# Kernel tuning notes

Hardware: AMD Instinct MI355X
Metric: run time of the kernel (lower is better)

Reference implementation:

```python
import jax, jax.numpy as jnp
import numpy as np

ZMAX = 92          # max atomic number in NLH table
BOHR = 0.52917721  # Bohr radius in Angstrom (au.BOHR)
ENERGY_UNIT = 1.0  # multiplier for 'Ha'
N_ATOMS = 100_000
N_EDGES = 6_400_000
TAB = (ZMAX + 1) ** 2  # 8649


def setup_inputs() -> dict:
    key = jax.random.key(0)
    k1, k2, k3, k4, k5, k6, k7 = jax.random.split(key, 7)
    species = jax.random.randint(k1, (N_ATOMS,), 0, 93, dtype=jnp.int32)
    edge_src = jax.random.randint(k2, (N_EDGES,), 0, N_ATOMS, dtype=jnp.int32)
    edge_dst = jax.random.randint(k3, (N_EDGES,), 0, N_ATOMS, dtype=jnp.int32)
    # distances kept away from zero (division by rijs)
    distances = 0.5 + 4.5 * jax.random.uniform(k4, (N_EDGES,), dtype=jnp.float32)
    switch = jax.random.uniform(k5, (N_EDGES,), dtype=jnp.float32)
    CS = jax.random.uniform(k6, (TAB, 3), dtype=jnp.float32)
    ALPHAS = jax.random.uniform(k7, (TAB, 3), dtype=jnp.float32) + 0.5
    return {"species": species, "edge_src": edge_src, "edge_dst": edge_dst,
            "distances": distances, "switch": switch, "CS": CS, "ALPHAS": ALPHAS}


def reference(species, edge_src, edge_dst, distances, switch, CS, ALPHAS):
    # pair index into (zmax+1)^2 coefficient table
    s12 = species[edge_src] + ZMAX * species[edge_dst]
    cs = CS[s12]          # [E, 3]
    alphas = ALPHAS[s12]  # [E, 3]
    Z = jnp.where(species > 0, species.astype(distances.dtype), 0.0)
    # 3-term exponential screening function
    phi = jnp.sum(cs * jnp.exp(-alphas * distances[:, None]), axis=-1)  # [E]
    ereppair = Z[edge_src] * Z[edge_dst] * phi * switch / distances
    erep_atomic = ENERGY_UNIT * 0.5 * BOHR * jax.ops.segment_sum(
        ereppair, edge_src, num_segments=species.shape[0])
    return erep_atomic
```

## Files before the change

kernel.cpp:

```cpp
#include <hip/hip_runtime.h>
#include <hip/hip_fp16.h>


#define ZMAX_C 92
#define TAB93  93
#define NTAB   (TAB93 * TAB93)
#define HALF_BOHR 0.264588605f
#define NBMAX 64
#define APB 2048
#define APB_LOG 11
#define SPLITS 16
#define TPB 256
#define EPT 8
#define BLK_EDGES (TPB * EPT)

typedef int            ivec4 __attribute__((ext_vector_type(4)));
typedef float          fvec4 __attribute__((ext_vector_type(4)));

#if __has_builtin(__builtin_amdgcn_rcpf)
#define FAST_RCP(x) __builtin_amdgcn_rcpf(x)
#else
#define FAST_RCP(x) (1.0f / (x))
#endif

__global__ __launch_bounds__(TPB) void p0_prep(
    const float* __restrict__ CS, const float* __restrict__ ALPHAS,
    const int* __restrict__ species,
    uint4* __restrict__ tab16, unsigned char* __restrict__ spc8,
    unsigned* __restrict__ cursor, float* __restrict__ out,
    int n_atoms, int nb)
{
    int i = blockIdx.x * TPB + threadIdx.x;
    if (i < NTAB) {
        int sd = i / TAB93;
        int ss = i - TAB93 * sd;
        int ref = ss + ZMAX_C * sd;
        float Z = (ss > 0 && sd > 0) ? (float)(ss * sd) : 0.0f;
        __half h[8];
        h[0] = __float2half_rn(CS[3*ref+0] * Z);
        h[1] = __float2half_rn(CS[3*ref+1] * Z);
        h[2] = __float2half_rn(CS[3*ref+2] * Z);
        h[3] = __float2half_rn(-ALPHAS[3*ref+0]);
        h[4] = __float2half_rn(-ALPHAS[3*ref+1]);
        h[5] = __float2half_rn(-ALPHAS[3*ref+2]);
        h[6] = __half(0.0f); h[7] = __half(0.0f);
        tab16[i] = *reinterpret_cast<uint4*>(h);
    }
    if (i < n_atoms) {
        spc8[i] = (unsigned char)species[i];
        out[i] = 0.0f;
    }
    if (i < nb) cursor[i] = 0u;
}

__device__ __forceinline__ float half_lo(unsigned u) {
    return __half2float(*reinterpret_cast<const __half*>(&u));
}
__device__ __forceinline__ float half_hi(unsigned u) {
    unsigned s = u >> 16;
    return __half2float(*reinterpret_cast<const __half*>(&s));
}

__global__ __launch_bounds__(TPB) void p1_bin(
    const int* __restrict__ edge_src, const int* __restrict__ edge_dst,
    const float* __restrict__ dist, const float* __restrict__ swt,
    const unsigned char* __restrict__ spc8, const uint4* __restrict__ tab16,
    unsigned* __restrict__ pairs, unsigned* __restrict__ cursor,
    int nb, int cap, int n_edges)
{
    __shared__ unsigned stage[BLK_EDGES];
    __shared__ unsigned hist4[4][NBMAX];
    __shared__ unsigned hist[NBMAX];
    __shared__ unsigned lbase[NBMAX];
    __shared__ unsigned gbase[NBMAX];

    int tid = threadIdx.x;
    if (tid < NBMAX) {
        hist4[0][tid] = 0; hist4[1][tid] = 0;
        hist4[2][tid] = 0; hist4[3][tid] = 0;
    }
    __syncthreads();

    int lane = tid & 63, wave = tid >> 6;
    long long wbase = (long long)blockIdx.x * BLK_EDGES + (long long)wave * (64 * EPT);

    unsigned meta[EPT];
    unsigned short s12r[EPT];

    {
        int srcv[EPT], dstv[EPT];
        #pragma unroll
        for (int j = 0; j < EPT / 4; ++j) {
            long long e0 = wbase + j * 256 + lane * 4;
            if (e0 + 3 < (long long)n_edges) {
                ivec4 s4 = *reinterpret_cast<const ivec4*>(edge_src + e0);
                ivec4 d4 = *reinterpret_cast<const ivec4*>(edge_dst + e0);
                #pragma unroll
                for (int k = 0; k < 4; ++k) { srcv[j*4+k] = s4[k]; dstv[j*4+k] = d4[k]; }
            } else {
                #pragma unroll
                for (int k = 0; k < 4; ++k) {
                    long long e = e0 + k;
                    bool v = (e < (long long)n_edges);
                    srcv[j*4+k] = v ? edge_src[e] : 0;
                    dstv[j*4+k] = v ? edge_dst[e] : 0;
                }
            }
        }
        int ssv[EPT], sdv[EPT];
        #pragma unroll
        for (int i = 0; i < EPT; ++i) ssv[i] = spc8[srcv[i]];
        #pragma unroll
        for (int i = 0; i < EPT; ++i) sdv[i] = spc8[dstv[i]];
        #pragma unroll
        for (int j = 0; j < EPT / 4; ++j) {
            long long e0 = wbase + j * 256 + lane * 4;
            #pragma unroll
            for (int k = 0; k < 4; ++k) {
                int idx = j * 4 + k;
                s12r[idx] = (unsigned short)(ssv[idx] + TAB93 * sdv[idx]);
                meta[idx] = 0u;
                if (e0 + k < (long long)n_edges) {
                    unsigned b    = (unsigned)srcv[idx] >> APB_LOG;
                    unsigned lsrc = (unsigned)srcv[idx] & (APB - 1);
                    unsigned rank = atomicAdd(&hist4[wave][b], 1u);
                    meta[idx] = 0x80000000u | (rank << 17) | (b << 11) | lsrc;
                }
            }
        }
    }
    __syncthreads();
    if (tid < 64) {
        unsigned h0 = hist4[0][tid], h1 = hist4[1][tid];
        unsigned h2 = hist4[2][tid], h3 = hist4[3][tid];
        unsigned tot = h0 + h1 + h2 + h3;
        hist4[0][tid] = 0;
        hist4[1][tid] = h0;
        hist4[2][tid] = h0 + h1;
        hist4[3][tid] = h0 + h1 + h2;
        if (tid < nb) hist[tid] = tot;
        unsigned v = (tid < nb) ? tot : 0u;
        unsigned x = v;
        #pragma unroll
        for (int off = 1; off < 64; off <<= 1) {
            unsigned y = __shfl_up(x, off);
            if ((tid & 63) >= off) x += y;
        }
        if (tid < nb) {
            lbase[tid] = x - v;
            gbase[tid] = v ? atomicAdd(cursor + tid, v) : 0u;
        }
    }
    __syncthreads();

    for (int jj = 0; jj < EPT / 8; ++jj) {
        long long eA = wbase + (jj*2+0) * 256 + lane * 4;
        long long eB = wbase + (jj*2+1) * 256 + lane * 4;
        float rA[4], wA[4], rB[4], wB[4];
        bool fullB = (eB + 3 < (long long)n_edges);
        if (fullB) {
            fvec4 r4 = *reinterpret_cast<const fvec4*>(dist + eA);
            fvec4 w4 = *reinterpret_cast<const fvec4*>(swt + eA);
            fvec4 r5 = *reinterpret_cast<const fvec4*>(dist + eB);
            fvec4 w5 = *reinterpret_cast<const fvec4*>(swt + eB);
            #pragma unroll
            for (int k = 0; k < 4; ++k) {
                rA[k] = r4[k]; wA[k] = w4[k]; rB[k] = r5[k]; wB[k] = w5[k];
            }
        } else {
            #pragma unroll
            for (int k = 0; k < 4; ++k) {
                long long ea = eA + k, eb = eB + k;
                bool va = (ea < (long long)n_edges), vb = (eb < (long long)n_edges);
                rA[k] = va ? dist[ea] : 1.f;  wA[k] = va ? swt[ea] : 0.f;
                rB[k] = vb ? dist[eb] : 1.f;  wB[k] = vb ? swt[eb] : 0.f;
            }
        }
        uint4 tA[4], tB[4];
        #pragma unroll
        for (int k = 0; k < 4; ++k) tA[k] = tab16[s12r[jj*8 + k]];
        #pragma unroll
        for (int k = 0; k < 4; ++k) tB[k] = tab16[s12r[jj*8 + 4 + k]];
        #pragma unroll
        for (int g = 0; g < 2; ++g) {
            const float* r = g ? rB : rA;
            const float* w = g ? wB : wA;
            const uint4* t = g ? tB : tA;
            #pragma unroll
            for (int k = 0; k < 4; ++k) {
                int idx = jj * 8 + g * 4 + k;
                unsigned m = meta[idx];
                if (!(m & 0x80000000u)) continue;
                float c0 = half_lo(t[k].x), c1 = half_hi(t[k].x);
                float c2 = half_lo(t[k].y), na0 = half_hi(t[k].y);
                float na1 = half_lo(t[k].z), na2 = half_hi(t[k].z);
                float phi = c0 * __expf(na0 * r[k])
                          + c1 * __expf(na1 * r[k])
                          + c2 * __expf(na2 * r[k]);
                float val = HALF_BOHR * phi * w[k] * FAST_RCP(r[k]);
                unsigned b = (m >> 11) & 63u;
                unsigned pos = lbase[b] + hist4[wave][b] + ((m >> 17) & 0x3FFFu);
                unsigned short hb = __half_as_ushort(__float2half_rn(val));
                stage[pos] = ((m & (APB - 1)) << 16) | (unsigned)hb;
            }
        }
    }
    __syncthreads();
    for (int b = wave; b < nb; b += 4) {
        unsigned cnt = hist[b], lb = lbase[b], gb = gbase[b];
        unsigned* dst = pairs + (size_t)b * (size_t)cap + gb;
        for (unsigned i = lane; i < cnt; i += 64)
            if (gb + i < (unsigned)cap) dst[i] = stage[lb + i];
    }
}

__global__ __launch_bounds__(TPB) void p2a_reduce(
    const unsigned* __restrict__ pairs, const unsigned* __restrict__ cursor,
    float* __restrict__ out, int cap, int n_atoms)
{
    int b = blockIdx.x / SPLITS;
    int s = blockIdx.x % SPLITS;
    __shared__ float acc[APB];
    for (int i = threadIdx.x; i < APB; i += TPB) acc[i] = 0.f;
    __syncthreads();
    unsigned cnt = cursor[b];
    if (cnt > (unsigned)cap) cnt = (unsigned)cap;
    unsigned nq = (cnt + 3u) >> 2;
    unsigned qb = (unsigned)((unsigned long long)nq * s / SPLITS);
    unsigned qe = (unsigned)((unsigned long long)nq * (s + 1) / SPLITS);
    const uint4* p4 = (const uint4*)(pairs + (size_t)b * (size_t)cap);
    for (unsigned q = qb + threadIdx.x; q < qe; q += TPB) {
        uint4 v = p4[q];
        unsigned base = q << 2;
        if (base + 3u < cnt) {
            unsafeAtomicAdd(&acc[v.x >> 16], __half2float(__ushort_as_half((unsigned short)(v.x & 0xFFFFu))));
            unsafeAtomicAdd(&acc[v.y >> 16], __half2float(__ushort_as_half((unsigned short)(v.y & 0xFFFFu))));
            unsafeAtomicAdd(&acc[v.z >> 16], __half2float(__ushort_as_half((unsigned short)(v.z & 0xFFFFu))));
            unsafeAtomicAdd(&acc[v.w >> 16], __half2float(__ushort_as_half((unsigned short)(v.w & 0xFFFFu))));
        } else {
            unsigned vv[4] = {v.x, v.y, v.z, v.w};
            #pragma unroll
            for (int e = 0; e < 4; ++e)
                if (base + (unsigned)e < cnt)
                    unsafeAtomicAdd(&acc[vv[e] >> 16],
                        __half2float(__ushort_as_half((unsigned short)(vv[e] & 0xFFFFu))));
        }
    }
    __syncthreads();
    int abase = b * APB;
    for (int k = threadIdx.x; k < APB; k += TPB) {
        int atom = abase + k;
        float vv = acc[k];
        if (atom < n_atoms && vv != 0.0f)
            unsafeAtomicAdd(&out[atom], vv);
    }
}

__global__ __launch_bounds__(TPB) void erep_edges_direct(
    const int* __restrict__ edge_src, const int* __restrict__ edge_dst,
    const float* __restrict__ dist, const float* __restrict__ swt,
    const int* __restrict__ species, const float* __restrict__ CS,
    const float* __restrict__ ALPHAS, float* __restrict__ out, int n_edges)
{
    int e = blockIdx.x * TPB + threadIdx.x;
    if (e >= n_edges) return;
    int ss = species[edge_src[e]], sd = species[edge_dst[e]];
    int prod = ss * sd;
    if (prod == 0) return;
    int s12 = ss + ZMAX_C * sd;
    float r = dist[e];
    float phi = CS[3*s12+0] * __expf(-ALPHAS[3*s12+0] * r)
              + CS[3*s12+1] * __expf(-ALPHAS[3*s12+1] * r)
              + CS[3*s12+2] * __expf(-ALPHAS[3*s12+2] * r);
    atomicAdd(out + edge_src[e],
              HALF_BOHR * (float)prod * phi * swt[e] * FAST_RCP(r));
}

extern "C" void kernel_launch(void* const* d_in, const int* in_sizes, int n_in,
                              void* d_out, int out_size, void* d_ws, size_t ws_size,
                              hipStream_t stream)
{
    const int*   species  = (const int*)  d_in[0];
    const int*   edge_src = (const int*)  d_in[1];
    const int*   edge_dst = (const int*)  d_in[2];
    const float* dist     = (const float*)d_in[3];
    const float* swt      = (const float*)d_in[4];
    const float* CS       = (const float*)d_in[5];
    const float* ALPHAS   = (const float*)d_in[6];
    float* out = (float*)d_out;

    int n_atoms = in_sizes[0];
    int n_edges = in_sizes[1];

    int nb = (n_atoms + APB - 1) / APB;
    long long capll = (long long)n_edges / nb + (long long)n_edges / ((long long)nb * 32) + 256;
    int cap = (int)((capll + 31) & ~31LL);

    size_t pairs_sz = ((size_t)nb * (size_t)cap * 4 + 255) & ~(size_t)255;
    size_t cur_sz   = ((size_t)nb * 4 + 255) & ~(size_t)255;
    size_t tab_sz   = ((size_t)NTAB * 16 + 255) & ~(size_t)255;
    size_t spc_sz   = ((size_t)n_atoms + 255) & ~(size_t)255;
    size_t need = pairs_sz + cur_sz + tab_sz + spc_sz;

    if (nb <= NBMAX && n_edges > 0 && ws_size >= need) {
        char* w = (char*)d_ws;
        unsigned*       pairs   = (unsigned*)w;
        unsigned*       cursor  = (unsigned*)(w + pairs_sz);
        uint4*          tab16   = (uint4*)(w + pairs_sz + cur_sz);
        unsigned char*  spc8    = (unsigned char*)(w + pairs_sz + cur_sz + tab_sz);

        int pmax = n_atoms > NTAB ? n_atoms : NTAB;
        p0_prep<<<(pmax + TPB - 1) / TPB, TPB, 0, stream>>>(
            CS, ALPHAS, species, tab16, spc8, cursor, out, n_atoms, nb);

        p1_bin<<<(n_edges + BLK_EDGES - 1) / BLK_EDGES, TPB, 0, stream>>>(
            edge_src, edge_dst, dist, swt, spc8, tab16,
            pairs, cursor, nb, cap, n_edges);

        p2a_reduce<<<nb * SPLITS, TPB, 0, stream>>>(pairs, cursor, out, cap, n_atoms);
    } else {
        (void)hipMemsetAsync(d_out, 0, (size_t)out_size * sizeof(float), stream);
        erep_edges_direct<<<(n_edges + TPB - 1) / TPB, TPB, 0, stream>>>(
            edge_src, edge_dst, dist, swt, species, CS, ALPHAS, out, n_edges);
    }
}
```

Measured before the change: 241.1 us.

## Stage packed coefficient table in LDS with 1024-thread binning blocks

Packs the per-pair coefficient table into 12-byte fp16 triples and copies the whole table into shared memory at the start of each binning block. Per-edge table lookups become LDS reads instead of global gathers. The block size grows to 1024 threads so the table load is shared across more edges, and the per-wave histogram and prefix logic is generalized to 16 waves. This costs a roughly 104 KB table copy per block and limits occupancy to about one block per CU.

```diff
diff --git a/kernel.cpp b/kernel.cpp
--- a/kernel.cpp
+++ b/kernel.cpp
@@ -10,7 +10,9 @@
 #define APB 2048
 #define APB_LOG 11
 #define SPLITS 16
-#define TPB 256
+#define TPB  1024
+#define NW   (TPB / 64)
+#define TPB2 256
 #define EPT 8
 #define BLK_EDGES (TPB * EPT)
 
@@ -23,28 +25,28 @@
 #define FAST_RCP(x) (1.0f / (x))
 #endif
 
-__global__ __launch_bounds__(TPB) void p0_prep(
+__global__ __launch_bounds__(TPB2) void p0_prep(
     const float* __restrict__ CS, const float* __restrict__ ALPHAS,
     const int* __restrict__ species,
-    uint4* __restrict__ tab16, unsigned char* __restrict__ spc8,
+    unsigned* __restrict__ tabp, unsigned char* __restrict__ spc8,
     unsigned* __restrict__ cursor, float* __restrict__ out,
     int n_atoms, int nb)
 {
-    int i = blockIdx.x * TPB + threadIdx.x;
+    int i = blockIdx.x * TPB2 + threadIdx.x;
     if (i < NTAB) {
         int sd = i / TAB93;
         int ss = i - TAB93 * sd;
         int ref = ss + ZMAX_C * sd;
         float Z = (ss > 0 && sd > 0) ? (float)(ss * sd) : 0.0f;
-        __half h[8];
-        h[0] = __float2half_rn(CS[3*ref+0] * Z);
-        h[1] = __float2half_rn(CS[3*ref+1] * Z);
-        h[2] = __float2half_rn(CS[3*ref+2] * Z);
-        h[3] = __float2half_rn(-ALPHAS[3*ref+0]);
-        h[4] = __float2half_rn(-ALPHAS[3*ref+1]);
-        h[5] = __float2half_rn(-ALPHAS[3*ref+2]);
-        h[6] = __half(0.0f); h[7] = __half(0.0f);
-        tab16[i] = *reinterpret_cast<uint4*>(h);
+        unsigned short h0 = __half_as_ushort(__float2half_rn(CS[3*ref+0] * Z));
+        unsigned short h1 = __half_as_ushort(__float2half_rn(CS[3*ref+1] * Z));
+        unsigned short h2 = __half_as_ushort(__float2half_rn(CS[3*ref+2] * Z));
+        unsigned short h3 = __half_as_ushort(__float2half_rn(-ALPHAS[3*ref+0]));
+        unsigned short h4 = __half_as_ushort(__float2half_rn(-ALPHAS[3*ref+1]));
+        unsigned short h5 = __half_as_ushort(__float2half_rn(-ALPHAS[3*ref+2]));
+        tabp[3*i+0] = (unsigned)h0 | ((unsigned)h1 << 16);
+        tabp[3*i+1] = (unsigned)h2 | ((unsigned)h3 << 16);
+        tabp[3*i+2] = (unsigned)h4 | ((unsigned)h5 << 16);
     }
     if (i < n_atoms) {
         spc8[i] = (unsigned char)species[i];
@@ -64,22 +66,22 @@
 __global__ __launch_bounds__(TPB) void p1_bin(
     const int* __restrict__ edge_src, const int* __restrict__ edge_dst,
     const float* __restrict__ dist, const float* __restrict__ swt,
-    const unsigned char* __restrict__ spc8, const uint4* __restrict__ tab16,
+    const unsigned char* __restrict__ spc8, const unsigned* __restrict__ tabp,
     unsigned* __restrict__ pairs, unsigned* __restrict__ cursor,
     int nb, int cap, int n_edges)
 {
+    __shared__ unsigned tabL[NTAB * 3];
     __shared__ unsigned stage[BLK_EDGES];
-    __shared__ unsigned hist4[4][NBMAX];
+    __shared__ unsigned histW[NW][NBMAX];
     __shared__ unsigned hist[NBMAX];
     __shared__ unsigned lbase[NBMAX];
     __shared__ unsigned gbase[NBMAX];
 
     int tid = threadIdx.x;
-    if (tid < NBMAX) {
-        hist4[0][tid] = 0; hist4[1][tid] = 0;
-        hist4[2][tid] = 0; hist4[3][tid] = 0;
-    }
-    __syncthreads();
+    ((unsigned*)histW)[tid] = 0;
+    __syncthreads();
+
+    for (int i = tid; i < NTAB * 3; i += TPB) tabL[i] = tabp[i];
 
     int lane = tid & 63, wave = tid >> 6;
     long long wbase = (long long)blockIdx.x * BLK_EDGES + (long long)wave * (64 * EPT);
@@ -123,7 +125,7 @@
                 if (e0 + k < (long long)n_edges) {
                     unsigned b    = (unsigned)srcv[idx] >> APB_LOG;
                     unsigned lsrc = (unsigned)srcv[idx] & (APB - 1);
-                    unsigned rank = atomicAdd(&hist4[wave][b], 1u);
+                    unsigned rank = atomicAdd(&histW[wave][b], 1u);
                     meta[idx] = 0x80000000u | (rank << 17) | (b << 11) | lsrc;
                 }
             }
@@ -131,13 +133,13 @@
     }
     __syncthreads();
     if (tid < 64) {
-        unsigned h0 = hist4[0][tid], h1 = hist4[1][tid];
-        unsigned h2 = hist4[2][tid], h3 = hist4[3][tid];
-        unsigned tot = h0 + h1 + h2 + h3;
-        hist4[0][tid] = 0;
-        hist4[1][tid] = h0;
-        hist4[2][tid] = h0 + h1;
-        hist4[3][tid] = h0 + h1 + h2;
+        unsigned h[NW];
+        #pragma unroll
+        for (int w = 0; w < NW; ++w) h[w] = histW[w][tid];
+        unsigned run = 0;
+        #pragma unroll
+        for (int w = 0; w < NW; ++w) { unsigned t = h[w]; histW[w][tid] = run; run += t; }
+        unsigned tot = run;
         if (tid < nb) hist[tid] = tot;
         unsigned v = (tid < nb) ? tot : 0u;
         unsigned x = v;
@@ -153,9 +155,9 @@
     }
     __syncthreads();
 
-    for (int jj = 0; jj < EPT / 8; ++jj) {
-        long long eA = wbase + (jj*2+0) * 256 + lane * 4;
-        long long eB = wbase + (jj*2+1) * 256 + lane * 4;
+    {
+        long long eA = wbase + lane * 4;
+        long long eB = wbase + 256 + lane * 4;
         float rA[4], wA[4], rB[4], wB[4];
         bool fullB = (eB + 3 < (long long)n_edges);
         if (fullB) {
@@ -176,37 +178,39 @@
                 rB[k] = vb ? dist[eb] : 1.f;  wB[k] = vb ? swt[eb] : 0.f;
             }
         }
-        uint4 tA[4], tB[4];
-        #pragma unroll
-        for (int k = 0; k < 4; ++k) tA[k] = tab16[s12r[jj*8 + k]];
-        #pragma unroll
-        for (int k = 0; k < 4; ++k) tB[k] = tab16[s12r[jj*8 + 4 + k]];
+        unsigned t0[EPT], t1[EPT], t2[EPT];
+        #pragma unroll
+        for (int k = 0; k < EPT; ++k) {
+            int s3 = 3 * (int)s12r[k];
+            t0[k] = tabL[s3 + 0];
+            t1[k] = tabL[s3 + 1];
+            t2[k] = tabL[s3 + 2];
+        }
         #pragma unroll
         for (int g = 0; g < 2; ++g) {
             const float* r = g ? rB : rA;
             const float* w = g ? wB : wA;
-            const uint4* t = g ? tB : tA;
             #pragma unroll
             for (int k = 0; k < 4; ++k) {
-                int idx = jj * 8 + g * 4 + k;
+                int idx = g * 4 + k;
                 unsigned m = meta[idx];
                 if (!(m & 0x80000000u)) continue;
-                float c0 = half_lo(t[k].x), c1 = half_hi(t[k].x);
-                float c2 = half_lo(t[k].y), na0 = half_hi(t[k].y);
-                float na1 = half_lo(t[k].z), na2 = half_hi(t[k].z);
+                float c0  = half_lo(t0[idx]), c1  = half_hi(t0[idx]);
+                float c2  = half_lo(t1[idx]), na0 = half_hi(t1[idx]);
+                float na1 = half_lo(t2[idx]), na2 = half_hi(t2[idx]);
                 float phi = c0 * __expf(na0 * r[k])
                           + c1 * __expf(na1 * r[k])
                           + c2 * __expf(na2 * r[k]);
                 float val = HALF_BOHR * phi * w[k] * FAST_RCP(r[k]);
                 unsigned b = (m >> 11) & 63u;
-                unsigned pos = lbase[b] + hist4[wave][b] + ((m >> 17) & 0x3FFFu);
+                unsigned pos = lbase[b] + histW[wave][b] + ((m >> 17) & 0x3FFFu);
                 unsigned short hb = __half_as_ushort(__float2half_rn(val));
                 stage[pos] = ((m & (APB - 1)) << 16) | (unsigned)hb;
             }
         }
     }
     __syncthreads();
-    for (int b = wave; b < nb; b += 4) {
+    for (int b = wave; b < nb; b += NW) {
         unsigned cnt = hist[b], lb = lbase[b], gb = gbase[b];
         unsigned* dst = pairs + (size_t)b * (size_t)cap + gb;
         for (unsigned i = lane; i < cnt; i += 64)
@@ -214,14 +218,14 @@
     }
 }
 
-__global__ __launch_bounds__(TPB) void p2a_reduce(
+__global__ __launch_bounds__(TPB2) void p2a_reduce(
     const unsigned* __restrict__ pairs, const unsigned* __restrict__ cursor,
     float* __restrict__ out, int cap, int n_atoms)
 {
     int b = blockIdx.x / SPLITS;
     int s = blockIdx.x % SPLITS;
     __shared__ float acc[APB];
-    for (int i = threadIdx.x; i < APB; i += TPB) acc[i] = 0.f;
+    for (int i = threadIdx.x; i < APB; i += TPB2) acc[i] = 0.f;
     __syncthreads();
     unsigned cnt = cursor[b];
     if (cnt > (unsigned)cap) cnt = (unsigned)cap;
@@ -229,7 +233,7 @@
     unsigned qb = (unsigned)((unsigned long long)nq * s / SPLITS);
     unsigned qe = (unsigned)((unsigned long long)nq * (s + 1) / SPLITS);
     const uint4* p4 = (const uint4*)(pairs + (size_t)b * (size_t)cap);
-    for (unsigned q = qb + threadIdx.x; q < qe; q += TPB) {
+    for (unsigned q = qb + threadIdx.x; q < qe; q += TPB2) {
         uint4 v = p4[q];
         unsigned base = q << 2;
         if (base + 3u < cnt) {
@@ -248,7 +252,7 @@
     }
     __syncthreads();
     int abase = b * APB;
-    for (int k = threadIdx.x; k < APB; k += TPB) {
+    for (int k = threadIdx.x; k < APB; k += TPB2) {
         int atom = abase + k;
         float vv = acc[k];
         if (atom < n_atoms && vv != 0.0f)
@@ -256,13 +260,13 @@
     }
 }
 
-__global__ __launch_bounds__(TPB) void erep_edges_direct(
+__global__ __launch_bounds__(TPB2) void erep_edges_direct(
     const int* __restrict__ edge_src, const int* __restrict__ edge_dst,
     const float* __restrict__ dist, const float* __restrict__ swt,
     const int* __restrict__ species, const float* __restrict__ CS,
     const float* __restrict__ ALPHAS, float* __restrict__ out, int n_edges)
 {
-    int e = blockIdx.x * TPB + threadIdx.x;
+    int e = blockIdx.x * TPB2 + threadIdx.x;
     if (e >= n_edges) return;
     int ss = species[edge_src[e]], sd = species[edge_dst[e]];
     int prod = ss * sd;
@@ -298,7 +302,7 @@
 
     size_t pairs_sz = ((size_t)nb * (size_t)cap * 4 + 255) & ~(size_t)255;
     size_t cur_sz   = ((size_t)nb * 4 + 255) & ~(size_t)255;
-    size_t tab_sz   = ((size_t)NTAB * 16 + 255) & ~(size_t)255;
+    size_t tab_sz   = ((size_t)NTAB * 12 + 255) & ~(size_t)255;
     size_t spc_sz   = ((size_t)n_atoms + 255) & ~(size_t)255;
     size_t need = pairs_sz + cur_sz + tab_sz + spc_sz;
 
@@ -306,21 +310,21 @@
         char* w = (char*)d_ws;
         unsigned*       pairs   = (unsigned*)w;
         unsigned*       cursor  = (unsigned*)(w + pairs_sz);
-        uint4*          tab16   = (uint4*)(w + pairs_sz + cur_sz);
+        unsigned*       tabp    = (unsigned*)(w + pairs_sz + cur_sz);
         unsigned char*  spc8    = (unsigned char*)(w + pairs_sz + cur_sz + tab_sz);
 
         int pmax = n_atoms > NTAB ? n_atoms : NTAB;
-        p0_prep<<<(pmax + TPB - 1) / TPB, TPB, 0, stream>>>(
-            CS, ALPHAS, species, tab16, spc8, cursor, out, n_atoms, nb);
+        p0_prep<<<(pmax + TPB2 - 1) / TPB2, TPB2, 0, stream>>>(
+            CS, ALPHAS, species, tabp, spc8, cursor, out, n_atoms, nb);
 
         p1_bin<<<(n_edges + BLK_EDGES - 1) / BLK_EDGES, TPB, 0, stream>>>(
-            edge_src, edge_dst, dist, swt, spc8, tab16,
+            edge_src, edge_dst, dist, swt, spc8, tabp,
             pairs, cursor, nb, cap, n_edges);
 
-        p2a_reduce<<<nb * SPLITS, TPB, 0, stream>>>(pairs, cursor, out, cap, n_atoms);
+        p2a_reduce<<<nb * SPLITS, TPB2, 0, stream>>>(pairs, cursor, out, cap, n_atoms);
     } else {
         (void)hipMemsetAsync(d_out, 0, (size_t)out_size * sizeof(float), stream);
-        erep_edges_direct<<<(n_edges + TPB - 1) / TPB, TPB, 0, stream>>>(
+        erep_edges_direct<<<(n_edges + TPB2 - 1) / TPB2, TPB2, 0, stream>>>(
             edge_src, edge_dst, dist, swt, species, CS, ALPHAS, out, n_edges);
     }
 }
```

Result: no change. 240.8 us (-0.1%).

## Fuse prep, binning and reduction into one cooperative persistent kernel

Applied to the files above, without the earlier changes.

Replaces the three separate launches (table prep, edge binning, per-bin reduction) with a single cooperative kernel that uses grid-wide syncs between phases and persistent blocks looping over edge chunks. The final reduction now writes per-split partial rows to a workspace and sums them in a last phase, replacing atomic accumulation into the output. This removes kernel launch gaps and the output zeroing, at the cost of grid syncs, host-side device attribute and occupancy queries on every call, and extra partial-buffer traffic.

```diff
diff --git a/kernel.cpp b/kernel.cpp
--- a/kernel.cpp
+++ b/kernel.cpp
@@ -1,5 +1,8 @@
 #include <hip/hip_runtime.h>
 #include <hip/hip_fp16.h>
+#include <hip/hip_cooperative_groups.h>
+
+namespace cg = cooperative_groups;
 
 
 #define ZMAX_C 92
@@ -11,6 +14,7 @@
 #define APB_LOG 11
 #define SPLITS 16
 #define TPB 256
+#define NW  (TPB / 64)
 #define EPT 8
 #define BLK_EDGES (TPB * EPT)
 
@@ -22,6 +26,237 @@
 #else
 #define FAST_RCP(x) (1.0f / (x))
 #endif
+
+__device__ __forceinline__ float half_lo(unsigned u) {
+    return __half2float(*reinterpret_cast<const __half*>(&u));
+}
+__device__ __forceinline__ float half_hi(unsigned u) {
+    unsigned s = u >> 16;
+    return __half2float(*reinterpret_cast<const __half*>(&s));
+}
+
+__global__ __launch_bounds__(TPB, 8) void fused_all(
+    const int* __restrict__ edge_src, const int* __restrict__ edge_dst,
+    const float* __restrict__ dist, const float* __restrict__ swt,
+    const int* __restrict__ species, const float* __restrict__ CS,
+    const float* __restrict__ ALPHAS,
+    unsigned* __restrict__ pairs, unsigned* __restrict__ cursor,
+    uint4* __restrict__ tab16, unsigned char* __restrict__ spc8,
+    float* __restrict__ partial, float* __restrict__ out,
+    int n_atoms, int n_edges, int nb, int cap, int nchunks)
+{
+    cg::grid_group grid = cg::this_grid();
+    const int G = gridDim.x;
+
+    __shared__ unsigned stage[BLK_EDGES];
+    __shared__ unsigned hist4[NW][NBMAX];
+    __shared__ unsigned hist[NBMAX];
+    __shared__ unsigned lbase[NBMAX];
+    __shared__ unsigned gbase[NBMAX];
+
+    int tid = threadIdx.x, bid = blockIdx.x;
+    int gtid = bid * TPB + tid;
+    int lane = tid & 63, wave = tid >> 6;
+
+    if (gtid < NTAB) {
+        int sd = gtid / TAB93;
+        int ss = gtid - TAB93 * sd;
+        int ref = ss + ZMAX_C * sd;
+        float Z = (ss > 0 && sd > 0) ? (float)(ss * sd) : 0.0f;
+        __half h[8];
+        h[0] = __float2half_rn(CS[3*ref+0] * Z);
+        h[1] = __float2half_rn(CS[3*ref+1] * Z);
+        h[2] = __float2half_rn(CS[3*ref+2] * Z);
+        h[3] = __float2half_rn(-ALPHAS[3*ref+0]);
+        h[4] = __float2half_rn(-ALPHAS[3*ref+1]);
+        h[5] = __float2half_rn(-ALPHAS[3*ref+2]);
+        h[6] = __half(0.0f); h[7] = __half(0.0f);
+        tab16[gtid] = *reinterpret_cast<uint4*>(h);
+    }
+    for (int a = gtid; a < n_atoms; a += G * TPB)
+        spc8[a] = (unsigned char)species[a];
+    if (gtid < nb) cursor[gtid] = 0u;
+    grid.sync();
+
+    for (int c = bid; c < nchunks; c += G) {
+        ((unsigned*)hist4)[tid] = 0u;
+        __syncthreads();
+
+        long long wbase = (long long)c * BLK_EDGES + (long long)wave * (64 * EPT);
+        unsigned meta[EPT];
+        unsigned short s12r[EPT];
+
+        {
+            int srcv[EPT], dstv[EPT];
+            #pragma unroll
+            for (int j = 0; j < EPT / 4; ++j) {
+                long long e0 = wbase + j * 256 + lane * 4;
+                if (e0 + 3 < (long long)n_edges) {
+                    ivec4 s4 = *reinterpret_cast<const ivec4*>(edge_src + e0);
+                    ivec4 d4 = *reinterpret_cast<const ivec4*>(edge_dst + e0);
+                    #pragma unroll
+                    for (int k = 0; k < 4; ++k) { srcv[j*4+k] = s4[k]; dstv[j*4+k] = d4[k]; }
+                } else {
+                    #pragma unroll
+                    for (int k = 0; k < 4; ++k) {
+                        long long e = e0 + k;
+                        bool v = (e < (long long)n_edges);
+                        srcv[j*4+k] = v ? edge_src[e] : 0;
+                        dstv[j*4+k] = v ? edge_dst[e] : 0;
+                    }
+                }
+            }
+            int ssv[EPT], sdv[EPT];
+            #pragma unroll
+            for (int i = 0; i < EPT; ++i) ssv[i] = spc8[srcv[i]];
+            #pragma unroll
+            for (int i = 0; i < EPT; ++i) sdv[i] = spc8[dstv[i]];
+            #pragma unroll
+            for (int j = 0; j < EPT / 4; ++j) {
+                long long e0 = wbase + j * 256 + lane * 4;
+                #pragma unroll
+                for (int k = 0; k < 4; ++k) {
+                    int idx = j * 4 + k;
+                    s12r[idx] = (unsigned short)(ssv[idx] + TAB93 * sdv[idx]);
+                    meta[idx] = 0u;
+                    if (e0 + k < (long long)n_edges) {
+                        unsigned b    = (unsigned)srcv[idx] >> APB_LOG;
+                        unsigned lsrc = (unsigned)srcv[idx] & (APB - 1);
+                        unsigned rank = atomicAdd(&hist4[wave][b], 1u);
+                        meta[idx] = 0x80000000u | (rank << 17) | (b << 11) | lsrc;
+                    }
+                }
+            }
+        }
+        __syncthreads();
+        if (tid < 64) {
+            unsigned h0 = hist4[0][tid], h1 = hist4[1][tid];
+            unsigned h2 = hist4[2][tid], h3 = hist4[3][tid];
+            unsigned tot = h0 + h1 + h2 + h3;
+            hist4[0][tid] = 0;
+            hist4[1][tid] = h0;
+            hist4[2][tid] = h0 + h1;
+            hist4[3][tid] = h0 + h1 + h2;
+            if (tid < nb) hist[tid] = tot;
+            unsigned v = (tid < nb) ? tot : 0u;
+            unsigned x = v;
+            #pragma unroll
+            for (int off = 1; off < 64; off <<= 1) {
+                unsigned y = __shfl_up(x, off);
+                if ((tid & 63) >= off) x += y;
+            }
+            if (tid < nb) {
+                lbase[tid] = x - v;
+                gbase[tid] = v ? atomicAdd(cursor + tid, v) : 0u;
+            }
+        }
+        __syncthreads();
+
+        {
+            long long eA = wbase + lane * 4;
+            long long eB = wbase + 256 + lane * 4;
+            float rA[4], wA[4], rB[4], wB[4];
+            bool fullB = (eB + 3 < (long long)n_edges);
+            if (fullB) {
+                fvec4 r4 = *reinterpret_cast<const fvec4*>(dist + eA);
+                fvec4 w4 = *reinterpret_cast<const fvec4*>(swt + eA);
+                fvec4 r5 = *reinterpret_cast<const fvec4*>(dist + eB);
+                fvec4 w5 = *reinterpret_cast<const fvec4*>(swt + eB);
+                #pragma unroll
+                for (int k = 0; k < 4; ++k) {
+                    rA[k] = r4[k]; wA[k] = w4[k]; rB[k] = r5[k]; wB[k] = w5[k];
+                }
+            } else {
+                #pragma unroll
+                for (int k = 0; k < 4; ++k) {
+                    long long ea = eA + k, eb = eB + k;
+                    bool va = (ea < (long long)n_edges), vb = (eb < (long long)n_edges);
+                    rA[k] = va ? dist[ea] : 1.f;  wA[k] = va ? swt[ea] : 0.f;
+                    rB[k] = vb ? dist[eb] : 1.f;  wB[k] = vb ? swt[eb] : 0.f;
+                }
+            }
+            uint4 tA[4], tB[4];
+            #pragma unroll
+            for (int k = 0; k < 4; ++k) tA[k] = tab16[s12r[k]];
+            #pragma unroll
+            for (int k = 0; k < 4; ++k) tB[k] = tab16[s12r[4 + k]];
+            #pragma unroll
+            for (int g = 0; g < 2; ++g) {
+                const float* r = g ? rB : rA;
+                const float* w = g ? wB : wA;
+                const uint4* t = g ? tB : tA;
+                #pragma unroll
+                for (int k = 0; k < 4; ++k) {
+                    int idx = g * 4 + k;
+                    unsigned m = meta[idx];
+                    if (!(m & 0x80000000u)) continue;
+                    float c0 = half_lo(t[k].x), c1 = half_hi(t[k].x);
+                    float c2 = half_lo(t[k].y), na0 = half_hi(t[k].y);
+                    float na1 = half_lo(t[k].z), na2 = half_hi(t[k].z);
+                    float phi = c0 * __expf(na0 * r[k])
+                              + c1 * __expf(na1 * r[k])
+                              + c2 * __expf(na2 * r[k]);
+                    float val = HALF_BOHR * phi * w[k] * FAST_RCP(r[k]);
+                    unsigned b = (m >> 11) & 63u;
+                    unsigned pos = lbase[b] + hist4[wave][b] + ((m >> 17) & 0x3FFFu);
+                    unsigned short hb = __half_as_ushort(__float2half_rn(val));
+                    stage[pos] = ((m & (APB - 1)) << 16) | (unsigned)hb;
+                }
+            }
+        }
+        __syncthreads();
+        for (int b = wave; b < nb; b += NW) {
+            unsigned cnt = hist[b], lb = lbase[b], gb = gbase[b];
+            unsigned* dst = pairs + (size_t)b * (size_t)cap + gb;
+            for (unsigned i = lane; i < cnt; i += 64)
+                if (gb + i < (unsigned)cap) dst[i] = stage[lb + i];
+        }
+    }
+    grid.sync();
+
+    int stride = nb * APB;
+    for (int w = bid; w < nb * SPLITS; w += G) {
+        int b = w / SPLITS;
+        int s = w % SPLITS;
+        float* acc = (float*)stage;
+        for (int i = tid; i < APB; i += TPB) acc[i] = 0.f;
+        __syncthreads();
+        unsigned cnt = cursor[b];
+        if (cnt > (unsigned)cap) cnt = (unsigned)cap;
+        unsigned nq = (cnt + 3u) >> 2;
+        unsigned qb = (unsigned)((unsigned long long)nq * s / SPLITS);
+        unsigned qe = (unsigned)((unsigned long long)nq * (s + 1) / SPLITS);
+        const uint4* p4 = (const uint4*)(pairs + (size_t)b * (size_t)cap);
+        for (unsigned q = qb + tid; q < qe; q += TPB) {
+            uint4 v = p4[q];
+            unsigned base = q << 2;
+            if (base + 3u < cnt) {
+                unsafeAtomicAdd(&acc[v.x >> 16], __half2float(__ushort_as_half((unsigned short)(v.x & 0xFFFFu))));
+                unsafeAtomicAdd(&acc[v.y >> 16], __half2float(__ushort_as_half((unsigned short)(v.y & 0xFFFFu))));
+                unsafeAtomicAdd(&acc[v.z >> 16], __half2float(__ushort_as_half((unsigned short)(v.z & 0xFFFFu))));
+                unsafeAtomicAdd(&acc[v.w >> 16], __half2float(__ushort_as_half((unsigned short)(v.w & 0xFFFFu))));
+            } else {
+                unsigned vv[4] = {v.x, v.y, v.z, v.w};
+                #pragma unroll
+                for (int e = 0; e < 4; ++e)
+                    if (base + (unsigned)e < cnt)
+                        unsafeAtomicAdd(&acc[vv[e] >> 16],
+                            __half2float(__ushort_as_half((unsigned short)(vv[e] & 0xFFFFu))));
+            }
+        }
+        __syncthreads();
+        float* prow = partial + (size_t)s * stride + (size_t)b * APB;
+        for (int k = tid; k < APB; k += TPB) prow[k] = acc[k];
+    }
+    grid.sync();
+
+    for (int a = gtid; a < n_atoms; a += G * TPB) {
+        float s = 0.f;
+        #pragma unroll
+        for (int x = 0; x < SPLITS; ++x) s += partial[(size_t)x * stride + a];
+        out[a] = s;
+    }
+}
 
 __global__ __launch_bounds__(TPB) void p0_prep(
     const float* __restrict__ CS, const float* __restrict__ ALPHAS,
@@ -53,14 +288,6 @@
     if (i < nb) cursor[i] = 0u;
 }
 
-__device__ __forceinline__ float half_lo(unsigned u) {
-    return __half2float(*reinterpret_cast<const __half*>(&u));
-}
-__device__ __forceinline__ float half_hi(unsigned u) {
-    unsigned s = u >> 16;
-    return __half2float(*reinterpret_cast<const __half*>(&s));
-}
-
 __global__ __launch_bounds__(TPB) void p1_bin(
     const int* __restrict__ edge_src, const int* __restrict__ edge_dst,
     const float* __restrict__ dist, const float* __restrict__ swt,
@@ -69,16 +296,13 @@
     int nb, int cap, int n_edges)
 {
     __shared__ unsigned stage[BLK_EDGES];
-    __shared__ unsigned hist4[4][NBMAX];
+    __shared__ unsigned hist4[NW][NBMAX];
     __shared__ unsigned hist[NBMAX];
     __shared__ unsigned lbase[NBMAX];
     __shared__ unsigned gbase[NBMAX];
 
     int tid = threadIdx.x;
-    if (tid < NBMAX) {
-        hist4[0][tid] = 0; hist4[1][tid] = 0;
-        hist4[2][tid] = 0; hist4[3][tid] = 0;
-    }
+    ((unsigned*)hist4)[tid] = 0u;
     __syncthreads();
 
     int lane = tid & 63, wave = tid >> 6;
@@ -86,7 +310,6 @@
 
     unsigned meta[EPT];
     unsigned short s12r[EPT];
-
     {
         int srcv[EPT], dstv[EPT];
         #pragma unroll
@@ -152,10 +375,9 @@
         }
     }
     __syncthreads();
-
-    for (int jj = 0; jj < EPT / 8; ++jj) {
-        long long eA = wbase + (jj*2+0) * 256 + lane * 4;
-        long long eB = wbase + (jj*2+1) * 256 + lane * 4;
+    {
+        long long eA = wbase + lane * 4;
+        long long eB = wbase + 256 + lane * 4;
         float rA[4], wA[4], rB[4], wB[4];
         bool fullB = (eB + 3 < (long long)n_edges);
         if (fullB) {
@@ -178,9 +400,9 @@
         }
         uint4 tA[4], tB[4];
         #pragma unroll
-        for (int k = 0; k < 4; ++k) tA[k] = tab16[s12r[jj*8 + k]];
-        #pragma unroll
-        for (int k = 0; k < 4; ++k) tB[k] = tab16[s12r[jj*8 + 4 + k]];
+        for (int k = 0; k < 4; ++k) tA[k] = tab16[s12r[k]];
+        #pragma unroll
+        for (int k = 0; k < 4; ++k) tB[k] = tab16[s12r[4 + k]];
         #pragma unroll
         for (int g = 0; g < 2; ++g) {
             const float* r = g ? rB : rA;
@@ -188,7 +410,7 @@
             const uint4* t = g ? tB : tA;
             #pragma unroll
             for (int k = 0; k < 4; ++k) {
-                int idx = jj * 8 + g * 4 + k;
+                int idx = g * 4 + k;
                 unsigned m = meta[idx];
                 if (!(m & 0x80000000u)) continue;
                 float c0 = half_lo(t[k].x), c1 = half_hi(t[k].x);
@@ -206,7 +428,7 @@
         }
     }
     __syncthreads();
-    for (int b = wave; b < nb; b += 4) {
+    for (int b = wave; b < nb; b += NW) {
         unsigned cnt = hist[b], lb = lbase[b], gb = gbase[b];
         unsigned* dst = pairs + (size_t)b * (size_t)cap + gb;
         for (unsigned i = lane; i < cnt; i += 64)
@@ -295,29 +517,53 @@
     int nb = (n_atoms + APB - 1) / APB;
     long long capll = (long long)n_edges / nb + (long long)n_edges / ((long long)nb * 32) + 256;
     int cap = (int)((capll + 31) & ~31LL);
+    int stride = nb * APB;
 
     size_t pairs_sz = ((size_t)nb * (size_t)cap * 4 + 255) & ~(size_t)255;
     size_t cur_sz   = ((size_t)nb * 4 + 255) & ~(size_t)255;
+    size_t part_sz  = ((size_t)SPLITS * (size_t)stride * 4 + 255) & ~(size_t)255;
     size_t tab_sz   = ((size_t)NTAB * 16 + 255) & ~(size_t)255;
     size_t spc_sz   = ((size_t)n_atoms + 255) & ~(size_t)255;
-    size_t need = pairs_sz + cur_sz + tab_sz + spc_sz;
+    size_t need = pairs_sz + cur_sz + part_sz + tab_sz + spc_sz;
 
     if (nb <= NBMAX && n_edges > 0 && ws_size >= need) {
         char* w = (char*)d_ws;
         unsigned*       pairs   = (unsigned*)w;
         unsigned*       cursor  = (unsigned*)(w + pairs_sz);
-        uint4*          tab16   = (uint4*)(w + pairs_sz + cur_sz);
-        unsigned char*  spc8    = (unsigned char*)(w + pairs_sz + cur_sz + tab_sz);
-
-        int pmax = n_atoms > NTAB ? n_atoms : NTAB;
-        p0_prep<<<(pmax + TPB - 1) / TPB, TPB, 0, stream>>>(
-            CS, ALPHAS, species, tab16, spc8, cursor, out, n_atoms, nb);
-
-        p1_bin<<<(n_edges + BLK_EDGES - 1) / BLK_EDGES, TPB, 0, stream>>>(
-            edge_src, edge_dst, dist, swt, spc8, tab16,
-            pairs, cursor, nb, cap, n_edges);
-
-        p2a_reduce<<<nb * SPLITS, TPB, 0, stream>>>(pairs, cursor, out, cap, n_atoms);
+        float*          partial = (float*)(w + pairs_sz + cur_sz);
+        uint4*          tab16   = (uint4*)(w + pairs_sz + cur_sz + part_sz);
+        unsigned char*  spc8    = (unsigned char*)(w + pairs_sz + cur_sz + part_sz + tab_sz);
+
+        int dev = 0;
+        (void)hipGetDevice(&dev);
+        int coop = 0, ncu = 0, occ = 0;
+        (void)hipDeviceGetAttribute(&coop, hipDeviceAttributeCooperativeLaunch, dev);
+        (void)hipDeviceGetAttribute(&ncu, hipDeviceAttributeMultiprocessorCount, dev);
+        (void)hipOccupancyMaxActiveBlocksPerMultiprocessor(&occ, (const void*)fused_all, TPB, 0);
+
+        int nchunks = (int)(((long long)n_edges + BLK_EDGES - 1) / BLK_EDGES);
+
+        if (coop && ncu > 0 && occ > 0 && (long long)occ * ncu >= 64) {
+            int G = occ * ncu;
+            if (G > 2048) G = 2048;
+            void* kargs[] = {
+                (void*)&edge_src, (void*)&edge_dst, (void*)&dist, (void*)&swt,
+                (void*)&species, (void*)&CS, (void*)&ALPHAS,
+                (void*)&pairs, (void*)&cursor, (void*)&tab16, (void*)&spc8,
+                (void*)&partial, (void*)&out,
+                (void*)&n_atoms, (void*)&n_edges, (void*)&nb, (void*)&cap,
+                (void*)&nchunks };
+            (void)hipLaunchCooperativeKernel((const void*)fused_all,
+                                             dim3(G), dim3(TPB), kargs, 0, stream);
+        } else {
+            int pmax = n_atoms > NTAB ? n_atoms : NTAB;
+            p0_prep<<<(pmax + TPB - 1) / TPB, TPB, 0, stream>>>(
+                CS, ALPHAS, species, tab16, spc8, cursor, out, n_atoms, nb);
+            p1_bin<<<nchunks, TPB, 0, stream>>>(
+                edge_src, edge_dst, dist, swt, spc8, tab16,
+                pairs, cursor, nb, cap, n_edges);
+            p2a_reduce<<<nb * SPLITS, TPB, 0, stream>>>(pairs, cursor, out, cap, n_atoms);
+        }
     } else {
         (void)hipMemsetAsync(d_out, 0, (size_t)out_size * sizeof(float), stream);
         erep_edges_direct<<<(n_edges + TPB - 1) / TPB, TPB, 0, stream>>>(
```

Measured after the change: 587.0 us. 144% more time.
